# Optimization experiments

Hardware: AMD Instinct MI355X
Metric: run time of the kernel (lower is better)

## Reference

```python
import jax, jax.numpy as jnp
import numpy as np

H = 512  # hidden_size
IN = 512  # input_size


def setup_inputs() -> dict:
    key = jax.random.key(0)
    ks = jax.random.split(key, 11)
    s = 1.0 / np.sqrt(H)
    T, B = 512, 256
    return {
        "x": jax.random.normal(ks[0], (T, B, IN), jnp.float32),
        "h0": jnp.zeros((B, H), jnp.float32),
        "g0": jnp.zeros((B, H), jnp.float32),
        # torch nn.Linear convention: y = x @ W.T + b, W ~ U(-1/sqrt(fan_in), ..)
        "Wx": jax.random.uniform(ks[1], (4 * H, IN), jnp.float32, -s, s),
        "bx": jax.random.uniform(ks[2], (4 * H,), jnp.float32, -s, s),
        "Wh": jax.random.uniform(ks[3], (3 * H, H), jnp.float32, -s, s),
        "bh": jax.random.uniform(ks[4], (3 * H,), jnp.float32, -s, s),
        "Wgh": jax.random.uniform(ks[5], (3 * H, H), jnp.float32, -s, s),
        "bgh": jax.random.uniform(ks[6], (3 * H,), jnp.float32, -s, s),
        "Whd": jax.random.uniform(ks[7], (3 * H, H), jnp.float32, -s, s),
        "bhd": jax.random.uniform(ks[8], (3 * H,), jnp.float32, -s, s),
        "Wg": jax.random.uniform(ks[9], (2 * H, H), jnp.float32, -s, s),
        "bg": jax.random.uniform(ks[10], (2 * H,), jnp.float32, -s, s),
    }


def _split(a, n):
    return jnp.split(a, n, axis=-1)


def reference(x, h0, g0, Wx, bx, Wh, bh, Wgh, bgh, Whd, bhd, Wg, bg):
    def step(carry, x_t):
        h, g = carry
        x_z, x_r, x_h, x_u = _split(x_t @ Wx.T + bx, 4)
        h_z, h_r, h_u = _split(h @ Wh.T + bh, 3)
        g_z, g_r, g_u = _split(g @ Wgh.T + bgh, 3)
        z = jax.nn.sigmoid(x_z + h_z + g_z)
        r = jax.nn.sigmoid(x_r + h_r + g_r)
        u = jax.nn.sigmoid(x_u + h_u + g_u)
        h_new = (1 - z) * h + z * jnp.tanh(x_h + r * h + u * g)
        h_d = h_new - h
        g_z2, g_r2 = _split(g @ Wg.T + bg, 2)
        hd_z, hd_r, hd_g = _split(h_d @ Whd.T + bhd, 3)
        z2 = jax.nn.sigmoid(hd_z + g_z2)
        r2 = jax.nn.sigmoid(hd_r + g_r2)
        g_new = (1 - z2) * g + z2 * jnp.tanh(hd_g + r2 * g)
        return (h_new, g_new), h_new

    (h, g), hs = jax.lax.scan(step, (h0, g0), x)
    return hs, h[None], g[None]
```

## Files before the change

kernel.cpp:

```cpp
#include <hip/hip_runtime.h>

#define Tn 512
#define Bn 256
#define Hn 512
#define INn 512
#define TPB 512

typedef __attribute__((ext_vector_type(8))) short bf16x8;
typedef __attribute__((ext_vector_type(4))) float f32x4;

__device__ __forceinline__ unsigned short f2bf(float f) {
  unsigned int u = __float_as_uint(f);
  unsigned int r = (u + 0x7fffu + ((u >> 16) & 1u)) >> 16;
  return (unsigned short)r;
}
__device__ __forceinline__ float bf2f(unsigned short u) {
  return __uint_as_float(((unsigned int)u) << 16);
}

__device__ __forceinline__ float sigm(float x) { return 1.0f / (1.0f + __expf(-x)); }
__device__ __forceinline__ float tanh_f(float x) { return 2.0f / (1.0f + __expf(-2.0f * x)) - 1.0f; }

__device__ __forceinline__ bf16x8 ld8(const unsigned short* p) {
  return *reinterpret_cast<const bf16x8*>(p);
}

__device__ __forceinline__ unsigned long long ald8(const unsigned short* p) {
  return __hip_atomic_load((const unsigned long long*)p, __ATOMIC_RELAXED,
                           __HIP_MEMORY_SCOPE_AGENT);
}
__device__ __forceinline__ void ast4(unsigned short* p, unsigned int v) {
  __hip_atomic_store((unsigned int*)p, v, __ATOMIC_RELAXED, __HIP_MEMORY_SCOPE_AGENT);
}
__device__ __forceinline__ unsigned int aldf(const unsigned int* p) {
  return __hip_atomic_load(p, __ATOMIC_RELAXED, __HIP_MEMORY_SCOPE_AGENT);
}
__device__ __forceinline__ void astf(unsigned int* p, unsigned int v) {
  __hip_atomic_store(p, v, __ATOMIC_RELAXED, __HIP_MEMORY_SCOPE_AGENT);
}

__device__ __forceinline__ f32x4 mfma16(bf16x8 a, bf16x8 b, f32x4 c) {
  return __builtin_amdgcn_mfma_f32_16x16x32_bf16(a, b, c, 0, 0, 0);
}

__global__ __launch_bounds__(256) void cvt_kernel(const float* __restrict__ in,
                                                  unsigned short* __restrict__ out, int n) {
  const int stride = gridDim.x * blockDim.x * 4;
  for (int i = (blockIdx.x * blockDim.x + threadIdx.x) * 4; i < n; i += stride) {
    float4 v = *reinterpret_cast<const float4*>(in + i);
    ushort4 o;
    o.x = f2bf(v.x); o.y = f2bf(v.y); o.z = f2bf(v.z); o.w = f2bf(v.w);
    *reinterpret_cast<ushort4*>(out + i) = o;
  }
}

__global__ __launch_bounds__(256) void xp_gemm_kernel(
    const unsigned short* __restrict__ xb,
    const unsigned short* __restrict__ Wxb,
    const float* __restrict__ bx,
    const float* __restrict__ bh,
    const float* __restrict__ bgh,
    unsigned short* __restrict__ XPb) {
  const int m0 = blockIdx.x * 64;
  const int n0 = blockIdx.y * 64;
  const int wave = threadIdx.x >> 6;
  const int lane = threadIdx.x & 63;
  const int l15 = lane & 15;
  const int lk = (lane >> 4) * 8;
  const int ro = (wave >> 1) * 32;
  const int co = (wave & 1) * 32;
  const unsigned short* ap = xb + (size_t)(m0 + ro + l15) * INn + lk;
  const unsigned short* bp = Wxb + (size_t)(n0 + co + l15) * INn + lk;
  f32x4 acc[2][2] = {};
  for (int k = 0; k < INn; k += 32) {
    bf16x8 a0 = ld8(ap + k);
    bf16x8 a1 = ld8(ap + 16 * INn + k);
    bf16x8 w0 = ld8(bp + k);
    bf16x8 w1 = ld8(bp + 16 * INn + k);
    acc[0][0] = mfma16(a0, w0, acc[0][0]);
    acc[0][1] = mfma16(a0, w1, acc[0][1]);
    acc[1][0] = mfma16(a1, w0, acc[1][0]);
    acc[1][1] = mfma16(a1, w1, acc[1][1]);
  }
#pragma unroll
  for (int rt = 0; rt < 2; ++rt)
#pragma unroll
    for (int ct = 0; ct < 2; ++ct) {
      const int col = n0 + co + ct * 16 + l15;
      const int gate = col >> 9, jcol = col & 511;
      const int jb = jcol >> 4, jl = jcol & 15;
      float bias = bx[col];
      if (col < 1024) bias += bh[col] + bgh[col];
      else if (col >= 1536) bias += bh[col - 512] + bgh[col - 512];
#pragma unroll
      for (int r = 0; r < 4; ++r) {
        const int row = m0 + ro + rt * 16 + (lane >> 4) * 4 + r;
        const int ttl = row >> 8, bb = row & 255;
        XPb[(((size_t)ttl * 8 + (bb >> 5)) * 32 + jb) * 2048 +
            gate * 512 + (bb & 31) * 16 + jl] = f2bf(acc[rt][ct][r] + bias);
      }
    }
}

__device__ __forceinline__ void poll_flags(const unsigned int* f, unsigned int ep,
                                           int jblk) {
  const int lane = threadIdx.x & 63;
  const int w = threadIdx.x >> 6;
  const int src = (w << 2) + ((lane & 7) >> 1);
  if (src == jblk) return;
  const unsigned int* p = f + src;
  while (aldf(p) < ep) __builtin_amdgcn_s_sleep(1);
}

__device__ __forceinline__ void gather32(const unsigned short* src,
                                         unsigned short* dst, int b0) {
  const int lane = threadIdx.x & 63;
  const int w = threadIdx.x >> 6;
  const int c = (w << 3) + (lane & 7);
  const int r0 = (lane >> 3) << 2;
#pragma unroll
  for (int p = 0; p < 4; ++p) {
    const int rr = r0 + p;
    const unsigned short* s = src + (size_t)(b0 + rr) * Hn + c * 8;
    unsigned long long lo = ald8(s);
    unsigned long long hi = ald8(s + 4);
    char* d = (char*)dst + rr * 1024 + ((c * 16) ^ ((rr & 7) << 4));
    *(unsigned long long*)d = lo;
    *(unsigned long long*)(d + 8) = hi;
  }
}

__global__ __launch_bounds__(512, 1) void persist_kernel(
    const unsigned short* __restrict__ Whb,
    const unsigned short* __restrict__ Wghb,
    const unsigned short* __restrict__ Whdb,
    const unsigned short* __restrict__ Wgb,
    const unsigned short* __restrict__ XPb,
    const float* __restrict__ bhd,
    const float* __restrict__ bg,
    unsigned short* __restrict__ hb0,
    unsigned short* __restrict__ gb,
    unsigned short* __restrict__ hdb,
    float* __restrict__ g_master,
    const float* __restrict__ h0,
    const float* __restrict__ g0,
    float* __restrict__ hs,
    float* __restrict__ h_tail,
    float* __restrict__ g_tail,
    unsigned int* __restrict__ slab,
    int t0, int Tc) {
  __shared__ unsigned short Wh_l[48 * 512];
  __shared__ unsigned short As_h[32 * 512];
  __shared__ unsigned short As_B[32 * 512];
  __shared__ float pa[8][32][17];
  __shared__ unsigned short xp_ls[2][2048];

  const int tid = threadIdx.x;
  const int grp = blockIdx.x & 7;
  const int jblk = blockIdx.x >> 3;
  const int j0 = jblk * 16;
  const int b0 = grp * 32;
  const int wv = tid >> 6;
  const int lane = tid & 63;
  const int l15 = lane & 15;
  const int lk = (lane >> 4) * 8;
  unsigned int* FH = slab + grp * 64;
  unsigned int* FG = slab + grp * 64 + 32;

  for (int i = tid; i < 48 * 64; i += TPB) {
    const int rr = i >> 6, c = i & 63;
    const int grow = (rr >> 4) * 512 + j0 + (rr & 15);
    const int byte = rr * 1024 + ((c * 16) ^ ((rr & 7) << 4));
    *reinterpret_cast<uint4*>(reinterpret_cast<char*>(Wh_l) + byte) =
        *reinterpret_cast<const uint4*>(Whb + (size_t)grow * 512 + c * 8);
  }
  {
    const unsigned short* src = XPb + ((size_t)grp * 32 + jblk) * 2048;
    *(unsigned long long*)&xp_ls[0][tid * 4] =
        *(const unsigned long long*)(src + tid * 4);
  }

  const int bl_e = tid >> 4, jl_e = tid & 15;
  const int j_e = j0 + jl_e;
  const size_t o_e = (size_t)(b0 + bl_e) * Hn + j_e;
  float h_m = (t0 == 0) ? h0[o_e] : hs[(size_t)(t0 - 1) * (Bn * Hn) + o_e];
  float g_m = (t0 == 0) ? g0[o_e] : g_master[o_e];
  const float bz2 = bhd[j_e] + bg[j_e];
  const float br2 = bhd[512 + j_e] + bg[512 + j_e];
  const float bgc = bhd[1024 + j_e];
  const int xo = bl_e * 16 + jl_e;
  const int swzA = (l15 & 7) << 4;
  float z2p = 0.0f, r2p = 0.0f;

  gather32(hb0 + (size_t)(t0 & 1) * (Bn * Hn), As_h, b0);
  gather32(gb, As_B, b0);
  __syncthreads();
  {
    const unsigned short* As = (wv < 3) ? As_h : As_B;
    const unsigned short* bp =
        (wv < 3) ? nullptr
        : (wv < 6) ? Wghb + (size_t)((wv - 3) * 512 + j0 + l15) * Hn + lk
                   : Wgb + (size_t)((wv - 6) * 512 + j0 + l15) * Hn + lk;
    const int wrow = wv * 16 + l15;
    f32x4 acc0 = {}, acc1 = {};
#pragma unroll
    for (int kt = 0; kt < 16; ++kt) {
      const int k2 = (kt * 32 + lk) * 2;
      const int abyte = k2 ^ swzA;
      bf16x8 a0 = *reinterpret_cast<const bf16x8*>(
          reinterpret_cast<const char*>(As) + l15 * 1024 + abyte);
      bf16x8 a1 = *reinterpret_cast<const bf16x8*>(
          reinterpret_cast<const char*>(As) + (16 + l15) * 1024 + abyte);
      bf16x8 bw = (wv < 3)
          ? *reinterpret_cast<const bf16x8*>(
                reinterpret_cast<const char*>(Wh_l) + wrow * 1024 + (k2 ^ ((wrow & 7) << 4)))
          : ld8(bp + kt * 32);
      acc0 = mfma16(a0, bw, acc0);
      acc1 = mfma16(a1, bw, acc1);
    }
#pragma unroll
    for (int r = 0; r < 4; ++r) {
      pa[wv][(lane >> 4) * 4 + r][l15] = acc0[r];
      pa[wv][16 + (lane >> 4) * 4 + r][l15] = acc1[r];
    }
  }
  __syncthreads();
  {
    const float z = sigm(bf2f(xp_ls[0][xo]) + pa[0][bl_e][jl_e] + pa[3][bl_e][jl_e]);
    const float r = sigm(bf2f(xp_ls[0][512 + xo]) + pa[1][bl_e][jl_e] + pa[4][bl_e][jl_e]);
    const float u = sigm(bf2f(xp_ls[0][1536 + xo]) + pa[2][bl_e][jl_e] + pa[5][bl_e][jl_e]);
    const float cand = tanh_f(bf2f(xp_ls[0][1024 + xo]) + r * h_m + u * g_m);
    const float hn = (1.0f - z) * h_m + z * cand;
    const float hd = hn - h_m;
    hs[(size_t)t0 * (Bn * Hn) + o_e] = hn;
    const unsigned int hn_u = f2bf(hn), hd_u = f2bf(hd);
    const unsigned int hn_hi = (unsigned int)__shfl_down((int)hn_u, 1);
    const unsigned int hd_hi = (unsigned int)__shfl_down((int)hd_u, 1);
    if ((jl_e & 1) == 0) {
      ast4(hb0 + (size_t)((t0 + 1) & 1) * (Bn * Hn) + o_e, hn_u | (hn_hi << 16));
      ast4(hdb + o_e, hd_u | (hd_hi << 16));
    }
    z2p = pa[6][bl_e][jl_e];
    r2p = pa[7][bl_e][jl_e];
    h_m = hn;
  }
  __syncthreads();
  if (tid == 0) astf(FH + jblk, 1u);

  for (int tt = 0; tt < Tc; ++tt) {
    const int t = t0 + tt;

    poll_flags(FH, (unsigned int)(tt + 1), jblk);
    gather32(hb0 + (size_t)((t + 1) & 1) * (Bn * Hn), As_h, b0);
    gather32(hdb, As_B, b0);
    __syncthreads();
    if (wv < 3) {
      const int wrow = wv * 16 + l15;
      f32x4 acc0 = {}, acc1 = {};
#pragma unroll
      for (int kt = 0; kt < 16; ++kt) {
        const int k2 = (kt * 32 + lk) * 2;
        const int abyte = k2 ^ swzA;
        bf16x8 a0 = *reinterpret_cast<const bf16x8*>(
            reinterpret_cast<const char*>(As_h) + l15 * 1024 + abyte);
        bf16x8 a1 = *reinterpret_cast<const bf16x8*>(
            reinterpret_cast<const char*>(As_h) + (16 + l15) * 1024 + abyte);
        bf16x8 bw = *reinterpret_cast<const bf16x8*>(
            reinterpret_cast<const char*>(Wh_l) + wrow * 1024 + (k2 ^ ((wrow & 7) << 4)));
        acc0 = mfma16(a0, bw, acc0);
        acc1 = mfma16(a1, bw, acc1);
      }
#pragma unroll
      for (int r = 0; r < 4; ++r) {
        pa[wv][(lane >> 4) * 4 + r][l15] = acc0[r];
        pa[wv][16 + (lane >> 4) * 4 + r][l15] = acc1[r];
      }
    } else if (wv < 6) {
      const unsigned short* bp = Whdb + (size_t)((wv - 3) * 512 + j0 + l15) * Hn + lk;
      f32x4 acc0 = {}, acc1 = {};
#pragma unroll
      for (int kt = 0; kt < 16; ++kt) {
        const int k2 = (kt * 32 + lk) * 2;
        const int abyte = k2 ^ swzA;
        bf16x8 a0 = *reinterpret_cast<const bf16x8*>(
            reinterpret_cast<const char*>(As_B) + l15 * 1024 + abyte);
        bf16x8 a1 = *reinterpret_cast<const bf16x8*>(
            reinterpret_cast<const char*>(As_B) + (16 + l15) * 1024 + abyte);
        bf16x8 bw = ld8(bp + kt * 32);
        acc0 = mfma16(a0, bw, acc0);
        acc1 = mfma16(a1, bw, acc1);
      }
#pragma unroll
      for (int r = 0; r < 4; ++r) {
        pa[wv][(lane >> 4) * 4 + r][l15] = acc0[r];
        pa[wv][16 + (lane >> 4) * 4 + r][l15] = acc1[r];
      }
    } else if (tt + 1 < Tc) {
      const unsigned short* src =
          XPb + (((size_t)(tt + 1) * 8 + grp) * 32 + jblk) * 2048;
      for (int i = tid - 384; i < 512; i += 128)
        *(unsigned long long*)&xp_ls[(tt + 1) & 1][i * 4] =
            *(const unsigned long long*)(src + i * 4);
    }
    __syncthreads();
    {
      const float z2 = sigm(pa[3][bl_e][jl_e] + z2p + bz2);
      const float r2 = sigm(pa[4][bl_e][jl_e] + r2p + br2);
      const float gc = tanh_f(pa[5][bl_e][jl_e] + bgc + r2 * g_m);
      const float gn = (1.0f - z2) * g_m + z2 * gc;
      g_m = gn;
      if (t == Tn - 1) g_tail[o_e] = gn;
      const unsigned int gn_u = f2bf(gn);
      const unsigned int gn_hi = (unsigned int)__shfl_down((int)gn_u, 1);
      if ((jl_e & 1) == 0) ast4(gb + o_e, gn_u | (gn_hi << 16));
    }
    __syncthreads();
    if (tid == 0) astf(FG + jblk, (unsigned int)(tt + 1));

    if (tt + 1 >= Tc) break;

    poll_flags(FG, (unsigned int)(tt + 1), jblk);
    gather32(gb, As_B, b0);
    __syncthreads();
    if (wv < 5) {
      const unsigned short* bp =
          (wv < 3) ? Wghb + (size_t)(wv * 512 + j0 + l15) * Hn + lk
                   : Wgb + (size_t)((wv - 3) * 512 + j0 + l15) * Hn + lk;
      f32x4 acc0 = {}, acc1 = {};
#pragma unroll
      for (int kt = 0; kt < 16; ++kt) {
        const int k2 = (kt * 32 + lk) * 2;
        const int abyte = k2 ^ swzA;
        bf16x8 a0 = *reinterpret_cast<const bf16x8*>(
            reinterpret_cast<const char*>(As_B) + l15 * 1024 + abyte);
        bf16x8 a1 = *reinterpret_cast<const bf16x8*>(
            reinterpret_cast<const char*>(As_B) + (16 + l15) * 1024 + abyte);
        bf16x8 bw = ld8(bp + kt * 32);
        acc0 = mfma16(a0, bw, acc0);
        acc1 = mfma16(a1, bw, acc1);
      }
#pragma unroll
      for (int r = 0; r < 4; ++r) {
        pa[3 + wv][(lane >> 4) * 4 + r][l15] = acc0[r];
        pa[3 + wv][16 + (lane >> 4) * 4 + r][l15] = acc1[r];
      }
    }
    __syncthreads();
    {
      const int xb_ = (tt + 1) & 1;
      const float z = sigm(bf2f(xp_ls[xb_][xo]) + pa[0][bl_e][jl_e] + pa[3][bl_e][jl_e]);
      const float r = sigm(bf2f(xp_ls[xb_][512 + xo]) + pa[1][bl_e][jl_e] + pa[4][bl_e][jl_e]);
      const float u = sigm(bf2f(xp_ls[xb_][1536 + xo]) + pa[2][bl_e][jl_e] + pa[5][bl_e][jl_e]);
      const float cand = tanh_f(bf2f(xp_ls[xb_][1024 + xo]) + r * h_m + u * g_m);
      const float hn = (1.0f - z) * h_m + z * cand;
      const float hd = hn - h_m;
      hs[(size_t)(t + 1) * (Bn * Hn) + o_e] = hn;
      if (t + 1 == Tn - 1) h_tail[o_e] = hn;
      const unsigned int hn_u = f2bf(hn), hd_u = f2bf(hd);
      const unsigned int hn_hi = (unsigned int)__shfl_down((int)hn_u, 1);
      const unsigned int hd_hi = (unsigned int)__shfl_down((int)hd_u, 1);
      if ((jl_e & 1) == 0) {
        ast4(hb0 + (size_t)(t & 1) * (Bn * Hn) + o_e, hn_u | (hn_hi << 16));
        ast4(hdb + o_e, hd_u | (hd_hi << 16));
      }
      z2p = pa[6][bl_e][jl_e];
      r2p = pa[7][bl_e][jl_e];
      h_m = hn;
    }
    __syncthreads();
    if (tid == 0) astf(FH + jblk, (unsigned int)(tt + 2));
  }
  g_master[o_e] = g_m;
}

extern "C" void kernel_launch(void* const* d_in, const int* in_sizes, int n_in,
                              void* d_out, int out_size, void* d_ws, size_t ws_size,
                              hipStream_t stream) {
  const float* x   = (const float*)d_in[0];
  const float* h0  = (const float*)d_in[1];
  const float* g0  = (const float*)d_in[2];
  const float* Wx  = (const float*)d_in[3];
  const float* bx  = (const float*)d_in[4];
  const float* Wh  = (const float*)d_in[5];
  const float* bh  = (const float*)d_in[6];
  const float* Wgh = (const float*)d_in[7];
  const float* bgh = (const float*)d_in[8];
  const float* Whd = (const float*)d_in[9];
  const float* bhd = (const float*)d_in[10];
  const float* Wg  = (const float*)d_in[11];
  const float* bg  = (const float*)d_in[12];

  char* ws = (char*)d_ws;
  unsigned short* Whb  = (unsigned short*)(ws + 0);
  unsigned short* Wghb = (unsigned short*)(ws + 1572864);
  unsigned short* Whdb = (unsigned short*)(ws + 3145728);
  unsigned short* Wgb  = (unsigned short*)(ws + 4718592);
  unsigned short* Wxb  = (unsigned short*)(ws + 5767168);
  unsigned short* hb0  = (unsigned short*)(ws + 7864320);
  unsigned short* gb_  = (unsigned short*)(ws + 8388608);
  unsigned short* hdb  = (unsigned short*)(ws + 8650752);
  float* g_master      = (float*)(ws + 8912896);
  unsigned int* flags  = (unsigned int*)(ws + 9437184);
  const size_t FIXED = 9453568ULL;

  int Tc = 64;
  while (Tc > 1 && FIXED + (size_t)Tc * (262144ULL + 1048576ULL) > ws_size) Tc >>= 1;
  unsigned short* xb  = (unsigned short*)(ws + FIXED);
  unsigned short* XPb = (unsigned short*)(ws + FIXED + (size_t)Tc * 262144ULL);

  float* hs = (float*)d_out;
  float* h_tail = hs + (size_t)Tn * Bn * Hn;
  float* g_tail = h_tail + (size_t)Bn * Hn;

  hipMemsetAsync(flags, 0, 16384, stream);
  cvt_kernel<<<dim3(512), 256, 0, stream>>>(Wh, Whb, 1536 * 512);
  cvt_kernel<<<dim3(512), 256, 0, stream>>>(Wgh, Wghb, 1536 * 512);
  cvt_kernel<<<dim3(512), 256, 0, stream>>>(Whd, Whdb, 1536 * 512);
  cvt_kernel<<<dim3(512), 256, 0, stream>>>(Wg, Wgb, 1024 * 512);
  cvt_kernel<<<dim3(512), 256, 0, stream>>>(Wx, Wxb, 2048 * 512);
  cvt_kernel<<<dim3(128), 256, 0, stream>>>(h0, hb0, Bn * Hn);
  cvt_kernel<<<dim3(128), 256, 0, stream>>>(g0, gb_, Bn * Hn);

  const int nChunks = Tn / Tc;
  for (int c = 0; c < nChunks; ++c) {
    const int t0 = c * Tc;
    cvt_kernel<<<dim3(1024), 256, 0, stream>>>(x + (size_t)t0 * Bn * INn, xb,
                                               Tc * Bn * INn);
    xp_gemm_kernel<<<dim3(Tc * 4, 32), 256, 0, stream>>>(xb, Wxb, bx, bh, bgh, XPb);
    persist_kernel<<<dim3(256), dim3(TPB), 0, stream>>>(
        Whb, Wghb, Whdb, Wgb, XPb, bhd, bg, hb0, gb_, hdb, g_master, h0, g0,
        hs, h_tail, g_tail, flags + c * 512, t0, Tc);
  }
}
```

Before: 9.710 ms.

## Fuse input projection GEMM into persistent recurrent kernel and enlarge time chunks

Removes the separate xp_gemm kernel and the XPb staging buffer. Each persistent block now computes its own x-projection tile for step t+2, using waves 4-7 during the g-phase while waves 0-3 poll flags and gather g. The Wg matmul is consolidated onto one wave to free the others. The chunk size grows to up to 512 steps, cutting kernel launches and flag resets. This removes global round-trips for the projection and launch overhead, but puts more MFMA work on the recurrent critical path of each step.

Measured after the change: 9.635 ms. Within noise of the previous version (-0.8%).

```diff
diff --git a/kernel.cpp b/kernel.cpp
--- a/kernel.cpp
+++ b/kernel.cpp
@@ -54,52 +54,48 @@
   }
 }
 
-__global__ __launch_bounds__(256) void xp_gemm_kernel(
-    const unsigned short* __restrict__ xb,
-    const unsigned short* __restrict__ Wxb,
-    const float* __restrict__ bx,
-    const float* __restrict__ bh,
-    const float* __restrict__ bgh,
-    unsigned short* __restrict__ XPb) {
-  const int m0 = blockIdx.x * 64;
-  const int n0 = blockIdx.y * 64;
-  const int wave = threadIdx.x >> 6;
+__device__ __forceinline__ void xp_tile(const unsigned short* __restrict__ xb,
+                                        const unsigned short* __restrict__ Wxb,
+                                        unsigned short* dst, int tl, int b0,
+                                        int j0, int gate, float biasv) {
   const int lane = threadIdx.x & 63;
   const int l15 = lane & 15;
   const int lk = (lane >> 4) * 8;
-  const int ro = (wave >> 1) * 32;
-  const int co = (wave & 1) * 32;
-  const unsigned short* ap = xb + (size_t)(m0 + ro + l15) * INn + lk;
-  const unsigned short* bp = Wxb + (size_t)(n0 + co + l15) * INn + lk;
-  f32x4 acc[2][2] = {};
-  for (int k = 0; k < INn; k += 32) {
-    bf16x8 a0 = ld8(ap + k);
-    bf16x8 a1 = ld8(ap + 16 * INn + k);
-    bf16x8 w0 = ld8(bp + k);
-    bf16x8 w1 = ld8(bp + 16 * INn + k);
-    acc[0][0] = mfma16(a0, w0, acc[0][0]);
-    acc[0][1] = mfma16(a0, w1, acc[0][1]);
-    acc[1][0] = mfma16(a1, w0, acc[1][0]);
-    acc[1][1] = mfma16(a1, w1, acc[1][1]);
-  }
-#pragma unroll
-  for (int rt = 0; rt < 2; ++rt)
-#pragma unroll
-    for (int ct = 0; ct < 2; ++ct) {
-      const int col = n0 + co + ct * 16 + l15;
-      const int gate = col >> 9, jcol = col & 511;
-      const int jb = jcol >> 4, jl = jcol & 15;
-      float bias = bx[col];
-      if (col < 1024) bias += bh[col] + bgh[col];
-      else if (col >= 1536) bias += bh[col - 512] + bgh[col - 512];
-#pragma unroll
-      for (int r = 0; r < 4; ++r) {
-        const int row = m0 + ro + rt * 16 + (lane >> 4) * 4 + r;
-        const int ttl = row >> 8, bb = row & 255;
-        XPb[(((size_t)ttl * 8 + (bb >> 5)) * 32 + jb) * 2048 +
-            gate * 512 + (bb & 31) * 16 + jl] = f2bf(acc[rt][ct][r] + bias);
-      }
-    }
+  const unsigned short* ap = xb + ((size_t)tl * Bn + b0 + l15) * INn + lk;
+  const unsigned short* bp = Wxb + (size_t)(gate * 512 + j0 + l15) * INn + lk;
+  f32x4 acc0 = {}, acc1 = {};
+#pragma unroll
+  for (int kt = 0; kt < 16; ++kt) {
+    bf16x8 a0 = ld8(ap + kt * 32);
+    bf16x8 a1 = ld8(ap + 16 * INn + kt * 32);
+    bf16x8 bw = ld8(bp + kt * 32);
+    acc0 = mfma16(a0, bw, acc0);
+    acc1 = mfma16(a1, bw, acc1);
+  }
+#pragma unroll
+  for (int r = 0; r < 4; ++r) {
+    const int row = (lane >> 4) * 4 + r;
+    dst[gate * 512 + row * 16 + l15] = f2bf(acc0[r] + biasv);
+    dst[gate * 512 + (row + 16) * 16 + l15] = f2bf(acc1[r] + biasv);
+  }
+}
+
+__device__ __forceinline__ void gather32(const unsigned short* src,
+                                         unsigned short* dst, int b0) {
+  const int lane = threadIdx.x & 63;
+  const int w = threadIdx.x >> 6;
+  const int c = (w << 3) + (lane & 7);
+  const int r0 = (lane >> 3) << 2;
+#pragma unroll
+  for (int p = 0; p < 4; ++p) {
+    const int rr = r0 + p;
+    const unsigned short* s = src + (size_t)(b0 + rr) * Hn + c * 8;
+    unsigned long long lo = ald8(s);
+    unsigned long long hi = ald8(s + 4);
+    char* d = (char*)dst + rr * 1024 + ((c * 16) ^ ((rr & 7) << 4));
+    *(unsigned long long*)d = lo;
+    *(unsigned long long*)(d + 8) = hi;
+  }
 }
 
 __device__ __forceinline__ void poll_flags(const unsigned int* f, unsigned int ep,
@@ -112,30 +108,16 @@
   while (aldf(p) < ep) __builtin_amdgcn_s_sleep(1);
 }
 
-__device__ __forceinline__ void gather32(const unsigned short* src,
-                                         unsigned short* dst, int b0) {
-  const int lane = threadIdx.x & 63;
-  const int w = threadIdx.x >> 6;
-  const int c = (w << 3) + (lane & 7);
-  const int r0 = (lane >> 3) << 2;
-#pragma unroll
-  for (int p = 0; p < 4; ++p) {
-    const int rr = r0 + p;
-    const unsigned short* s = src + (size_t)(b0 + rr) * Hn + c * 8;
-    unsigned long long lo = ald8(s);
-    unsigned long long hi = ald8(s + 4);
-    char* d = (char*)dst + rr * 1024 + ((c * 16) ^ ((rr & 7) << 4));
-    *(unsigned long long*)d = lo;
-    *(unsigned long long*)(d + 8) = hi;
-  }
-}
-
 __global__ __launch_bounds__(512, 1) void persist_kernel(
     const unsigned short* __restrict__ Whb,
     const unsigned short* __restrict__ Wghb,
     const unsigned short* __restrict__ Whdb,
     const unsigned short* __restrict__ Wgb,
-    const unsigned short* __restrict__ XPb,
+    const unsigned short* __restrict__ xb,
+    const unsigned short* __restrict__ Wxb,
+    const float* __restrict__ bx,
+    const float* __restrict__ bh,
+    const float* __restrict__ bgh,
     const float* __restrict__ bhd,
     const float* __restrict__ bg,
     unsigned short* __restrict__ hb0,
@@ -174,11 +156,16 @@
     *reinterpret_cast<uint4*>(reinterpret_cast<char*>(Wh_l) + byte) =
         *reinterpret_cast<const uint4*>(Whb + (size_t)grow * 512 + c * 8);
   }
-  {
-    const unsigned short* src = XPb + ((size_t)grp * 32 + jblk) * 2048;
-    *(unsigned long long*)&xp_ls[0][tid * 4] =
-        *(const unsigned long long*)(src + tid * 4);
-  }
+
+  const int gx = wv & 3;
+  const int jx = j0 + l15;
+  float bxp = bx[gx * 512 + jx];
+  if (gx == 0) bxp += bh[jx] + bgh[jx];
+  else if (gx == 1) bxp += bh[512 + jx] + bgh[512 + jx];
+  else if (gx == 3) bxp += bh[1024 + jx] + bgh[1024 + jx];
+
+  if (wv < 4) xp_tile(xb, Wxb, &xp_ls[0][0], 0, b0, j0, gx, bxp);
+  else if (Tc > 1) xp_tile(xb, Wxb, &xp_ls[1][0], 1, b0, j0, gx, bxp);
 
   const int bl_e = tid >> 4, jl_e = tid & 15;
   const int j_e = j0 + jl_e;
@@ -295,12 +282,6 @@
         pa[wv][(lane >> 4) * 4 + r][l15] = acc0[r];
         pa[wv][16 + (lane >> 4) * 4 + r][l15] = acc1[r];
       }
-    } else if (tt + 1 < Tc) {
-      const unsigned short* src =
-          XPb + (((size_t)(tt + 1) * 8 + grp) * 32 + jblk) * 2048;
-      for (int i = tid - 384; i < 512; i += 128)
-        *(unsigned long long*)&xp_ls[(tt + 1) & 1][i * 4] =
-            *(const unsigned long long*)(src + i * 4);
     }
     __syncthreads();
     {
@@ -319,13 +300,30 @@
 
     if (tt + 1 >= Tc) break;
 
-    poll_flags(FG, (unsigned int)(tt + 1), jblk);
-    gather32(gb, As_B, b0);
-    __syncthreads();
-    if (wv < 5) {
-      const unsigned short* bp =
-          (wv < 3) ? Wghb + (size_t)(wv * 512 + j0 + l15) * Hn + lk
-                   : Wgb + (size_t)((wv - 3) * 512 + j0 + l15) * Hn + lk;
+    if (wv < 4) {
+      {
+        const int src = (wv << 3) + (lane & 7);
+        if (src != jblk) {
+          const unsigned int* p = FG + src;
+          while (aldf(p) < (unsigned int)(tt + 1)) __builtin_amdgcn_s_sleep(1);
+        }
+      }
+      for (int p = 0; p < 8; ++p) {
+        const int idx = tid + p * 256;
+        const int rr = idx >> 6, c = idx & 63;
+        const unsigned short* s = gb + (size_t)(b0 + rr) * Hn + c * 8;
+        unsigned long long lo = ald8(s);
+        unsigned long long hi = ald8(s + 4);
+        char* d = (char*)As_B + rr * 1024 + ((c * 16) ^ ((rr & 7) << 4));
+        *(unsigned long long*)d = lo;
+        *(unsigned long long*)(d + 8) = hi;
+      }
+    } else if (tt + 2 < Tc) {
+      xp_tile(xb, Wxb, &xp_ls[tt & 1][0], tt + 2, b0, j0, gx, bxp);
+    }
+    __syncthreads();
+    if (wv < 3) {
+      const unsigned short* bp = Wghb + (size_t)(wv * 512 + j0 + l15) * Hn + lk;
       f32x4 acc0 = {}, acc1 = {};
 #pragma unroll
       for (int kt = 0; kt < 16; ++kt) {
@@ -343,6 +341,32 @@
       for (int r = 0; r < 4; ++r) {
         pa[3 + wv][(lane >> 4) * 4 + r][l15] = acc0[r];
         pa[3 + wv][16 + (lane >> 4) * 4 + r][l15] = acc1[r];
+      }
+    } else if (wv == 3) {
+      const unsigned short* bp0 = Wgb + (size_t)(j0 + l15) * Hn + lk;
+      const unsigned short* bp1 = Wgb + (size_t)(512 + j0 + l15) * Hn + lk;
+      f32x4 a00 = {}, a01 = {}, a10 = {}, a11 = {};
+#pragma unroll
+      for (int kt = 0; kt < 16; ++kt) {
+        const int k2 = (kt * 32 + lk) * 2;
+        const int abyte = k2 ^ swzA;
+        bf16x8 a0 = *reinterpret_cast<const bf16x8*>(
+            reinterpret_cast<const char*>(As_B) + l15 * 1024 + abyte);
+        bf16x8 a1 = *reinterpret_cast<const bf16x8*>(
+            reinterpret_cast<const char*>(As_B) + (16 + l15) * 1024 + abyte);
+        bf16x8 w0 = ld8(bp0 + kt * 32);
+        bf16x8 w1 = ld8(bp1 + kt * 32);
+        a00 = mfma16(a0, w0, a00);
+        a10 = mfma16(a1, w0, a10);
+        a01 = mfma16(a0, w1, a01);
+        a11 = mfma16(a1, w1, a11);
+      }
+#pragma unroll
+      for (int r = 0; r < 4; ++r) {
+        pa[6][(lane >> 4) * 4 + r][l15] = a00[r];
+        pa[6][16 + (lane >> 4) * 4 + r][l15] = a10[r];
+        pa[7][(lane >> 4) * 4 + r][l15] = a01[r];
+        pa[7][16 + (lane >> 4) * 4 + r][l15] = a11[r];
       }
     }
     __syncthreads();
@@ -403,16 +427,14 @@
   unsigned int* flags  = (unsigned int*)(ws + 9437184);
   const size_t FIXED = 9453568ULL;
 
-  int Tc = 64;
-  while (Tc > 1 && FIXED + (size_t)Tc * (262144ULL + 1048576ULL) > ws_size) Tc >>= 1;
-  unsigned short* xb  = (unsigned short*)(ws + FIXED);
-  unsigned short* XPb = (unsigned short*)(ws + FIXED + (size_t)Tc * 262144ULL);
+  int Tc = 512;
+  while (Tc > 1 && FIXED + (size_t)Tc * 262144ULL > ws_size) Tc >>= 1;
+  unsigned short* xb = (unsigned short*)(ws + FIXED);
 
   float* hs = (float*)d_out;
   float* h_tail = hs + (size_t)Tn * Bn * Hn;
   float* g_tail = h_tail + (size_t)Bn * Hn;
 
-  hipMemsetAsync(flags, 0, 16384, stream);
   cvt_kernel<<<dim3(512), 256, 0, stream>>>(Wh, Whb, 1536 * 512);
   cvt_kernel<<<dim3(512), 256, 0, stream>>>(Wgh, Wghb, 1536 * 512);
   cvt_kernel<<<dim3(512), 256, 0, stream>>>(Whd, Whdb, 1536 * 512);
@@ -424,11 +446,11 @@
   const int nChunks = Tn / Tc;
   for (int c = 0; c < nChunks; ++c) {
     const int t0 = c * Tc;
-    cvt_kernel<<<dim3(1024), 256, 0, stream>>>(x + (size_t)t0 * Bn * INn, xb,
+    hipMemsetAsync(flags, 0, 2048, stream);
+    cvt_kernel<<<dim3(2048), 256, 0, stream>>>(x + (size_t)t0 * Bn * INn, xb,
                                                Tc * Bn * INn);
-    xp_gemm_kernel<<<dim3(Tc * 4, 32), 256, 0, stream>>>(xb, Wxb, bx, bh, bgh, XPb);
     persist_kernel<<<dim3(256), dim3(TPB), 0, stream>>>(
-        Whb, Wghb, Whdb, Wgb, XPb, bhd, bg, hb0, gb_, hdb, g_master, h0, g0,
-        hs, h_tail, g_tail, flags + c * 512, t0, Tc);
-  }
-}
+        Whb, Wghb, Whdb, Wgb, xb, Wxb, bx, bh, bgh, bhd, bg, hb0, gb_, hdb,
+        g_master, h0, g0, hs, h_tail, g_tail, flags, t0, Tc);
+  }
+}
```
